# Optimization experiments

Measured on AMD Instinct MI355X. Metric: run time of the kernel, lower is better.

The kernel has to match this reference:

```python
import jax, jax.numpy as jnp
import numpy as np

EPS = 1e-7  # K.epsilon()


def setup_inputs() -> dict:
    key = jax.random.key(0)
    k1, k2, k3, k4 = jax.random.split(key, 4)
    B, T, S = 512, 32, 2048  # batch, time_steps, seq_len
    inputs = jax.random.normal(k1, (B, T, S), dtype=jnp.float32)
    # Keras mask (float 0/1), same shape as inputs
    mask = (jax.random.uniform(k2, (B, T, S)) < 0.8).astype(jnp.float32)
    # 'uniform' keras initializer: U(-0.05, 0.05)
    W = jax.random.uniform(k3, (S, T, T), minval=-0.05, maxval=0.05, dtype=jnp.float32)
    b = jax.random.uniform(k4, (S, T), minval=-0.05, maxval=0.05, dtype=jnp.float32)
    return {"inputs": inputs, "mask": mask, "W": W, "b": b}


def reference(inputs, mask, W, b):
    # (B,T,S) -> (B,S,T), apply mask
    x = jnp.transpose(inputs, (0, 2, 1)) * jnp.transpose(mask, (0, 2, 1))
    # per-position matmul, batched over B and S (replaces the tf.scan over batch)
    z = jnp.einsum('bst,stu->bsu', x, W) + b  # (B,S,T)
    e = jnp.exp(jnp.tanh(z))
    att = e / (jnp.sum(e, axis=2, keepdims=True) + EPS)  # softmax-like over T
    return jnp.sum(att * x, axis=1)  # (B,T)
```

## Files before the change

kernel.cpp:

```cpp
#include <hip/hip_runtime.h>

#define EPS_K 1e-7f

typedef __attribute__((ext_vector_type(8))) short  frag8;
typedef __attribute__((ext_vector_type(16))) float accf16;

__device__ __forceinline__ unsigned f2bf(float f) {
  union { float f; unsigned u; } v; v.f = f;
  unsigned u = v.u;
  u += 0x7FFFu + ((u >> 16) & 1u);
  return u >> 16;
}

__device__ __forceinline__ float bf2f(unsigned short s) {
  union { unsigned u; float f; } v; v.u = ((unsigned)s) << 16;
  return v.f;
}

__device__ __forceinline__ int xidx(int b, int t, int s) {
  const int tp = t ^ ((b >> 3) & 3);
  const int sp = s ^ (2 * (b & 7));
  return b * 512 + tp * 16 + sp;
}

template <bool USE_WS>
__global__ __launch_bounds__(256, 4) void attn_fused(
    const float* __restrict__ inp,
    const float* __restrict__ msk,
    const float* __restrict__ Wt,
    const float* __restrict__ bias,
    float* __restrict__ part,
    float* __restrict__ out)
{
  __shared__ unsigned short x_us[32 * 512];

  const int tid = threadIdx.x;
  const int st  = blockIdx.x >> 4;
  const int bg  = blockIdx.x & 15;
  const int s0  = st * 16;

  {
    const int c  = tid & 3;
    const int t  = (tid >> 2) & 31;
    const int bh = tid >> 7;
    unsigned* x32 = (unsigned*)x_us;
    #pragma unroll 4
    for (int bs = 0; bs < 16; ++bs) {
      const int b = bh * 16 + bs;
      const int gidx = ((bg * 32 + b) * 32 + t) * 2048 + s0 + 4 * c;
      const float4 vi = *(const float4*)(inp + gidx);
      const float4 vm = *(const float4*)(msk + gidx);
      const int tp = t ^ ((b >> 3) & 3);
      const int k  = b & 7;
      const unsigned p0 = f2bf(vi.x * vm.x) | (f2bf(vi.y * vm.y) << 16);
      const unsigned p1 = f2bf(vi.z * vm.z) | (f2bf(vi.w * vm.w) << 16);
      const int base = b * 256 + tp * 8;
      x32[base + ((2 * c)     ^ k)] = p0;
      x32[base + ((2 * c + 1) ^ k)] = p1;
    }
  }
  __syncthreads();

  const int lane = tid & 63;
  const int wv   = tid >> 6;
  const int n    = lane & 31;
  const int h    = lane >> 5;

  float O[16];
  #pragma unroll
  for (int r = 0; r < 16; ++r) O[r] = 0.f;

  #pragma unroll
  for (int si = 0; si < 4; ++si) {
    const int sl = wv * 4 + si;
    const int s  = s0 + sl;
    const float* Wp = Wt + s * 1024;

    frag8 a1, a2, b1, b2;
    #pragma unroll
    for (int j = 0; j < 8; ++j) {
      const int t1 = 8 * h + j;
      a1[j] = (short)f2bf(Wp[t1 * 32 + n]);
      a2[j] = (short)f2bf(Wp[(t1 + 16) * 32 + n]);
      b1[j] = (short)x_us[xidx(n, t1, sl)];
      b2[j] = (short)x_us[xidx(n, t1 + 16, sl)];
    }

    accf16 acc;
    #pragma unroll
    for (int r = 0; r < 16; ++r) {
      const int u = (r & 3) + 8 * (r >> 2) + 4 * h;
      acc[r] = bias[s * 32 + u];
    }
    acc = __builtin_amdgcn_mfma_f32_32x32x16_bf16(a1, b1, acc, 0, 0, 0);
    acc = __builtin_amdgcn_mfma_f32_32x32x16_bf16(a2, b2, acc, 0, 0, 0);

    float e[16];
    float ps = 0.f;
    #pragma unroll
    for (int r = 0; r < 16; ++r) {
      const float z  = acc[r];
      const float e2 = __expf(2.f * z);
      const float th = 1.f - 2.f / (e2 + 1.f);
      e[r] = __expf(th);
      ps  += e[r];
    }
    const float tot = ps + __shfl_xor(ps, 32, 64);
    const float inv = 1.f / (tot + EPS_K);

    #pragma unroll
    for (int r = 0; r < 16; ++r) {
      const int u = (r & 3) + 8 * (r >> 2) + 4 * h;
      O[r] += e[r] * inv * bf2f(x_us[xidx(n, u, sl)]);
    }
  }

  __syncthreads();
  float* red = (float*)x_us;
  #pragma unroll
  for (int r = 0; r < 16; ++r) {
    const int u = (r & 3) + 8 * (r >> 2) + 4 * h;
    red[wv * 1024 + n * 32 + (u ^ n)] = O[r];
  }
  __syncthreads();

  const int q0 = tid * 4;
  float4 v;
  float* vp = (float*)&v;
  #pragma unroll
  for (int i = 0; i < 4; ++i) {
    const int q = q0 + i;
    const int b = q >> 5, u = q & 31;
    float sum = 0.f;
    #pragma unroll
    for (int w = 0; w < 4; ++w) sum += red[w * 1024 + b * 32 + (u ^ b)];
    vp[i] = sum;
  }
  if (USE_WS) {
    *(float4*)(part + (size_t)st * 16384 + bg * 1024 + q0) = v;
  } else {
    float* op = out + bg * 1024 + q0;
    #pragma unroll
    for (int i = 0; i < 4; ++i) atomicAdd(op + i, vp[i]);
  }
}

__global__ __launch_bounds__(256) void reduce_part(
    const float* __restrict__ part, float* __restrict__ out)
{
  const int f = blockIdx.x * 256 + threadIdx.x;
  float s = 0.f;
  #pragma unroll 8
  for (int st = 0; st < 128; ++st) s += part[(size_t)st * 16384 + f];
  out[f] = s;
}

extern "C" void kernel_launch(void* const* d_in, const int* in_sizes, int n_in,
                              void* d_out, int out_size, void* d_ws, size_t ws_size,
                              hipStream_t stream) {
  const float* inp  = (const float*)d_in[0];
  const float* msk  = (const float*)d_in[1];
  const float* Wt   = (const float*)d_in[2];
  const float* bias = (const float*)d_in[3];
  float* out = (float*)d_out;

  const size_t need = (size_t)128 * 16384 * sizeof(float);
  if (ws_size >= need) {
    attn_fused<true><<<dim3(128 * 16), dim3(256), 0, stream>>>(
        inp, msk, Wt, bias, (float*)d_ws, out);
    reduce_part<<<dim3(64), dim3(256), 0, stream>>>((const float*)d_ws, out);
  } else {
    hipMemsetAsync(out, 0, (size_t)out_size * sizeof(float), stream);
    attn_fused<false><<<dim3(128 * 16), dim3(256), 0, stream>>>(
        inp, msk, Wt, bias, nullptr, out);
  }
}
```

Before: 325.1 us.

## Pre-transpose W to bf16 and vectorize LDS layout for MFMA fragments

Adds a prep kernel that converts W to bf16 and transposes it per position, so the main kernel loads A fragments as single 16-byte vectors instead of scalar float loads with per-element conversion. The x staging in LDS is re-laid out with an XOR swizzle so that B fragments, epilogue x values and bias load as vectors instead of scalar shorts. Occupancy hint is raised from 4 to 5 blocks. The cost is an extra kernel launch and W round-trip through workspace on every call, plus larger workspace requirements.

```diff
diff --git a/kernel.cpp b/kernel.cpp
--- a/kernel.cpp
+++ b/kernel.cpp
@@ -2,8 +2,9 @@
 
 #define EPS_K 1e-7f
 
-typedef __attribute__((ext_vector_type(8))) short  frag8;
-typedef __attribute__((ext_vector_type(16))) float accf16;
+typedef __attribute__((ext_vector_type(8)))  short          frag8;
+typedef __attribute__((ext_vector_type(16))) float          accf16;
+typedef __attribute__((ext_vector_type(4)))  unsigned short us4;
 
 __device__ __forceinline__ unsigned f2bf(float f) {
   union { float f; unsigned u; } v; v.f = f;
@@ -11,23 +12,46 @@
   u += 0x7FFFu + ((u >> 16) & 1u);
   return u >> 16;
 }
-
 __device__ __forceinline__ float bf2f(unsigned short s) {
   union { unsigned u; float f; } v; v.u = ((unsigned)s) << 16;
   return v.f;
 }
-
-__device__ __forceinline__ int xidx(int b, int t, int s) {
-  const int tp = t ^ ((b >> 3) & 3);
-  const int sp = s ^ (2 * (b & 7));
-  return b * 512 + tp * 16 + sp;
-}
-
-template <bool USE_WS>
-__global__ __launch_bounds__(256, 4) void attn_fused(
+__device__ __forceinline__ unsigned pk_bf16(float lo, float hi) {
+  return f2bf(lo) | (f2bf(hi) << 16);
+}
+
+__global__ __launch_bounds__(256) void wbf_prep(
+    const float* __restrict__ Wt, unsigned short* __restrict__ Wbf)
+{
+  __shared__ unsigned short tile[32 * 33];
+  const int s   = blockIdx.x;
+  const int tid = threadIdx.x;
+  {
+    const int t  = tid >> 3;
+    const int uc = tid & 7;
+    const float4 v = *(const float4*)(Wt + s * 1024 + t * 32 + 4 * uc);
+    tile[t * 33 + 4 * uc + 0] = (unsigned short)f2bf(v.x);
+    tile[t * 33 + 4 * uc + 1] = (unsigned short)f2bf(v.y);
+    tile[t * 33 + 4 * uc + 2] = (unsigned short)f2bf(v.z);
+    tile[t * 33 + 4 * uc + 3] = (unsigned short)f2bf(v.w);
+  }
+  __syncthreads();
+  {
+    const int u  = tid >> 3;
+    const int tc = tid & 7;
+    uint2 d;
+    d.x = (unsigned)tile[(4 * tc + 0) * 33 + u] | ((unsigned)tile[(4 * tc + 1) * 33 + u] << 16);
+    d.y = (unsigned)tile[(4 * tc + 2) * 33 + u] | ((unsigned)tile[(4 * tc + 3) * 33 + u] << 16);
+    *(uint2*)(Wbf + s * 1024 + u * 32 + 4 * tc) = d;
+  }
+}
+
+template <bool WBF, bool USE_WS>
+__global__ __launch_bounds__(256, 5) void attn_fused(
     const float* __restrict__ inp,
     const float* __restrict__ msk,
     const float* __restrict__ Wt,
+    const unsigned short* __restrict__ Wbf,
     const float* __restrict__ bias,
     float* __restrict__ part,
     float* __restrict__ out)
@@ -39,24 +63,31 @@
   const int bg  = blockIdx.x & 15;
   const int s0  = st * 16;
 
-  {
-    const int c  = tid & 3;
-    const int t  = (tid >> 2) & 31;
-    const int bh = tid >> 7;
-    unsigned* x32 = (unsigned*)x_us;
-    #pragma unroll 4
-    for (int bs = 0; bs < 16; ++bs) {
-      const int b = bh * 16 + bs;
-      const int gidx = ((bg * 32 + b) * 32 + t) * 2048 + s0 + 4 * c;
-      const float4 vi = *(const float4*)(inp + gidx);
-      const float4 vm = *(const float4*)(msk + gidx);
-      const int tp = t ^ ((b >> 3) & 3);
-      const int k  = b & 7;
-      const unsigned p0 = f2bf(vi.x * vm.x) | (f2bf(vi.y * vm.y) << 16);
-      const unsigned p1 = f2bf(vi.z * vm.z) | (f2bf(vi.w * vm.w) << 16);
-      const int base = b * 256 + tp * 8;
-      x32[base + ((2 * c)     ^ k)] = p0;
-      x32[base + ((2 * c + 1) ^ k)] = p1;
+  #pragma unroll
+  for (int iter = 0; iter < 2; ++iter) {
+    const int idx = iter * 256 + tid;
+    const int sc  = idx & 3;
+    const int tb  = (idx >> 2) & 3;
+    const int b   = idx >> 4;
+    const float* ip = inp + ((size_t)(bg * 32 + b) * 32 + 8 * tb) * 2048 + s0 + 4 * sc;
+    const float* mp = msk + ((size_t)(bg * 32 + b) * 32 + 8 * tb) * 2048 + s0 + 4 * sc;
+    unsigned c32[4][4];
+    #pragma unroll
+    for (int j2 = 0; j2 < 4; ++j2) {
+      const float4 vi0 = *(const float4*)(ip + (2 * j2)     * 2048);
+      const float4 vm0 = *(const float4*)(mp + (2 * j2)     * 2048);
+      const float4 vi1 = *(const float4*)(ip + (2 * j2 + 1) * 2048);
+      const float4 vm1 = *(const float4*)(mp + (2 * j2 + 1) * 2048);
+      c32[0][j2] = pk_bf16(vi0.x * vm0.x, vi1.x * vm1.x);
+      c32[1][j2] = pk_bf16(vi0.y * vm0.y, vi1.y * vm1.y);
+      c32[2][j2] = pk_bf16(vi0.z * vm0.z, vi1.z * vm1.z);
+      c32[3][j2] = pk_bf16(vi0.w * vm0.w, vi1.w * vm1.w);
+    }
+    #pragma unroll
+    for (int w = 0; w < 4; ++w) {
+      const int L = tb * 16 + 4 * sc + w;
+      unsigned* dst = (unsigned*)(x_us + b * 512 + ((L ^ (b & 7)) * 8));
+      *(uint4*)dst = make_uint4(c32[w][0], c32[w][1], c32[w][2], c32[w][3]);
     }
   }
   __syncthreads();
@@ -65,6 +96,7 @@
   const int wv   = tid >> 6;
   const int n    = lane & 31;
   const int h    = lane >> 5;
+  const int nx   = n & 7;
 
   float O[16];
   #pragma unroll
@@ -74,23 +106,31 @@
   for (int si = 0; si < 4; ++si) {
     const int sl = wv * 4 + si;
     const int s  = s0 + sl;
-    const float* Wp = Wt + s * 1024;
-
-    frag8 a1, a2, b1, b2;
-    #pragma unroll
-    for (int j = 0; j < 8; ++j) {
-      const int t1 = 8 * h + j;
-      a1[j] = (short)f2bf(Wp[t1 * 32 + n]);
-      a2[j] = (short)f2bf(Wp[(t1 + 16) * 32 + n]);
-      b1[j] = (short)x_us[xidx(n, t1, sl)];
-      b2[j] = (short)x_us[xidx(n, t1 + 16, sl)];
-    }
+
+    frag8 a1, a2;
+    if (WBF) {
+      const unsigned short* wp = Wbf + s * 1024 + n * 32 + 8 * h;
+      a1 = *(const frag8*)(wp);
+      a2 = *(const frag8*)(wp + 16);
+    } else {
+      const float* Wp = Wt + s * 1024;
+      #pragma unroll
+      for (int j = 0; j < 8; ++j) {
+        const int t1 = 8 * h + j;
+        a1[j] = (short)f2bf(Wp[t1 * 32 + n]);
+        a2[j] = (short)f2bf(Wp[(t1 + 16) * 32 + n]);
+      }
+    }
+
+    const frag8 b1 = *(const frag8*)(x_us + n * 512 + (((h      * 16 + sl) ^ nx) * 8));
+    const frag8 b2 = *(const frag8*)(x_us + n * 512 + ((((h + 2) * 16 + sl) ^ nx) * 8));
 
     accf16 acc;
     #pragma unroll
-    for (int r = 0; r < 16; ++r) {
-      const int u = (r & 3) + 8 * (r >> 2) + 4 * h;
-      acc[r] = bias[s * 32 + u];
+    for (int g = 0; g < 4; ++g) {
+      const float4 bb = *(const float4*)(bias + s * 32 + 8 * g + 4 * h);
+      acc[4 * g + 0] = bb.x; acc[4 * g + 1] = bb.y;
+      acc[4 * g + 2] = bb.z; acc[4 * g + 3] = bb.w;
     }
     acc = __builtin_amdgcn_mfma_f32_32x32x16_bf16(a1, b1, acc, 0, 0, 0);
     acc = __builtin_amdgcn_mfma_f32_32x32x16_bf16(a2, b2, acc, 0, 0, 0);
@@ -109,9 +149,11 @@
     const float inv = 1.f / (tot + EPS_K);
 
     #pragma unroll
-    for (int r = 0; r < 16; ++r) {
-      const int u = (r & 3) + 8 * (r >> 2) + 4 * h;
-      O[r] += e[r] * inv * bf2f(x_us[xidx(n, u, sl)]);
+    for (int g = 0; g < 4; ++g) {
+      const us4 xv = *(const us4*)(x_us + n * 512 + (((g * 16 + sl) ^ nx) * 8) + 4 * h);
+      #pragma unroll
+      for (int i = 0; i < 4; ++i)
+        O[4 * g + i] += e[4 * g + i] * inv * bf2f(xv[i]);
     }
   }
 
@@ -164,14 +206,24 @@
   const float* bias = (const float*)d_in[3];
   float* out = (float*)d_out;
 
-  const size_t need = (size_t)128 * 16384 * sizeof(float);
-  if (ws_size >= need) {
-    attn_fused<true><<<dim3(128 * 16), dim3(256), 0, stream>>>(
-        inp, msk, Wt, bias, (float*)d_ws, out);
-    reduce_part<<<dim3(64), dim3(256), 0, stream>>>((const float*)d_ws, out);
+  const size_t part_sz = (size_t)128 * 16384 * sizeof(float);
+  const size_t wbf_sz  = (size_t)2048 * 1024 * sizeof(unsigned short);
+
+  if (ws_size >= part_sz + wbf_sz) {
+    float* part = (float*)d_ws;
+    unsigned short* Wbf = (unsigned short*)((char*)d_ws + part_sz);
+    wbf_prep<<<dim3(2048), dim3(256), 0, stream>>>(Wt, Wbf);
+    attn_fused<true, true><<<dim3(2048), dim3(256), 0, stream>>>(
+        inp, msk, Wt, Wbf, bias, part, out);
+    reduce_part<<<dim3(64), dim3(256), 0, stream>>>(part, out);
+  } else if (ws_size >= part_sz) {
+    float* part = (float*)d_ws;
+    attn_fused<false, true><<<dim3(2048), dim3(256), 0, stream>>>(
+        inp, msk, Wt, nullptr, bias, part, out);
+    reduce_part<<<dim3(64), dim3(256), 0, stream>>>(part, out);
   } else {
-    hipMemsetAsync(out, 0, (size_t)out_size * sizeof(float), stream);
-    attn_fused<false><<<dim3(128 * 16), dim3(256), 0, stream>>>(
-        inp, msk, Wt, bias, nullptr, out);
-  }
-}
+    (void)hipMemsetAsync(out, 0, (size_t)out_size * sizeof(float), stream);
+    attn_fused<false, false><<<dim3(2048), dim3(256), 0, stream>>>(
+        inp, msk, Wt, nullptr, bias, nullptr, out);
+  }
+}
```

Measured after the change: 311.3 us. 1.04x faster.
